# Kernel tuning notes

Measured on AMD Instinct MI355X. Metric: run time of the kernel, lower is better.

## Reference

```python
import jax, jax.numpy as jnp
import numpy as np

N = 100000   # nodes
E = 1250000  # edges
D = 64       # in = hidden = out channels
LN_EPS = 1e-5
L2_EPS = 1e-12


def setup_inputs() -> dict:
    key = jax.random.key(0)
    ks = jax.random.split(key, 16)
    s = 1.0 / np.sqrt(D)
    inp = {
        "x": jax.random.normal(ks[0], (N, D), jnp.float32),
        "edge_index": jax.random.randint(ks[1], (2, E), 0, N, dtype=jnp.int64),
    }
    for i in range(3):  # SAGEConv i: out = mean_aggr @ Wl + bl + x @ Wr
        inp[f"Wl{i}"] = jax.random.normal(ks[2 + 2 * i], (D, D), jnp.float32) * s
        inp[f"bl{i}"] = jnp.zeros((D,), jnp.float32)
        inp[f"Wr{i}"] = jax.random.normal(ks[3 + 2 * i], (D, D), jnp.float32) * s
    for i in range(2):  # LayerNorm after layers 0,1
        inp[f"g{i}"] = jnp.ones((D,), jnp.float32)
        inp[f"b{i}"] = jnp.zeros((D,), jnp.float32)
    return inp


def _sage_conv(x, src, dst, Wl, bl, Wr):
    # PyG SAGEConv(aggr='mean'): lin_l(mean of neighbor msgs) + lin_r(x)
    agg = jax.ops.segment_sum(x[src], dst, num_segments=N)          # [N, D]
    deg = jax.ops.segment_sum(jnp.ones((src.shape[0],), x.dtype), dst, num_segments=N)
    mean = agg / jnp.maximum(deg, 1.0)[:, None]
    return mean @ Wl + bl + x @ Wr


def _layer_norm(h, g, b):
    mu = jnp.mean(h, axis=-1, keepdims=True)
    var = jnp.mean((h - mu) ** 2, axis=-1, keepdims=True)
    return (h - mu) * jax.lax.rsqrt(var + LN_EPS) * g + b


def reference(x, edge_index, Wl0, bl0, Wr0, Wl1, bl1, Wr1, Wl2, bl2, Wr2, g0, b0, g1, b1):
    src, dst = edge_index[0], edge_index[1]
    Ws = [(Wl0, bl0, Wr0), (Wl1, bl1, Wr1), (Wl2, bl2, Wr2)]
    lns = [(g0, b0), (g1, b1)]
    h = x
    for i in range(3):
        res = h  # residual projections are Identity (equal dims)
        h = _sage_conv(h, src, dst, *Ws[i])
        if i < 2:
            h = _layer_norm(h, *lns[i])
            h = jax.nn.relu(h)
            h = h + res
            # dropout is identity in eval mode
        else:
            h = h + res
    # F.normalize(p=2, dim=1)
    nrm = jnp.sqrt(jnp.sum(h * h, axis=1, keepdims=True))
    return h / jnp.maximum(nrm, L2_EPS)
```

## Files before the change

### kernel.cpp

```cpp
#include <hip/hip_runtime.h>

#define DD   64
#define WSTR 136
#define BSH  9
#define BNODES 512
#define BCAPSH 13

typedef unsigned int uint32;
typedef __attribute__((ext_vector_type(8))) short short8;
typedef __attribute__((ext_vector_type(4))) float f32x4;

__device__ __forceinline__ unsigned short f2bf_rne(float f) {
    uint32 u = __float_as_uint(f);
    u += 0x7fffu + ((u >> 16) & 1u);
    return (unsigned short)(u >> 16);
}
__device__ __forceinline__ float bf_lo(uint32 w) { return __uint_as_float(w << 16); }
__device__ __forceinline__ float bf_hi(uint32 w) { return __uint_as_float(w & 0xffff0000u); }

__global__ __launch_bounds__(256) void cvt_kernel(const float* __restrict__ x,
                                                  unsigned short* __restrict__ xb,
                                                  int n4, int* __restrict__ gCnt) {
    if (blockIdx.x == 0 && threadIdx.x < 256) gCnt[threadIdx.x] = 0;
    int i = blockIdx.x * 256 + threadIdx.x;
    if (i < n4) {
        float4 v = ((const float4*)x)[i];
        ushort4 p;
        p.x = f2bf_rne(v.x); p.y = f2bf_rne(v.y);
        p.z = f2bf_rne(v.z); p.w = f2bf_rne(v.w);
        ((ushort4*)xb)[i] = p;
    }
}

__global__ __launch_bounds__(1024) void bucket_kernel(const int* __restrict__ src,
                                                      const int* __restrict__ dst,
                                                      int* __restrict__ gCnt,
                                                      int2* __restrict__ buf, int E) {
    __shared__ int ldsCnt[256];
    __shared__ int base[256];
    const int t = threadIdx.x;
    if (t < 256) ldsCnt[t] = 0;
    __syncthreads();

    const int e0 = blockIdx.x * 4096;
    int bk[4], rk[4], sv[4], dv[4];
#pragma unroll
    for (int k = 0; k < 4; ++k) {
        int e = e0 + k * 1024 + t;
        bk[k] = -1;
        if (e < E) {
            dv[k] = dst[e];
            sv[k] = src[e];
            bk[k] = dv[k] >> BSH;
            rk[k] = atomicAdd(&ldsCnt[bk[k]], 1);
        }
    }
    __syncthreads();
    if (t < 256 && ldsCnt[t] > 0) base[t] = atomicAdd(&gCnt[t], ldsCnt[t]);
    __syncthreads();
#pragma unroll
    for (int k = 0; k < 4; ++k) {
        if (bk[k] >= 0) {
            int pos = (bk[k] << BCAPSH) + base[bk[k]] + rk[k];
            buf[pos] = make_int2(sv[k], dv[k]);
        }
    }
}

__global__ __launch_bounds__(256) void scan_buckets(const int* __restrict__ gCnt,
                                                    int* __restrict__ csrBase, int NB) {
    __shared__ int s[256];
    int t = threadIdx.x;
    int v = (t < NB) ? gCnt[t] : 0;
    s[t] = v;
    __syncthreads();
    for (int d = 1; d < 256; d <<= 1) {
        int u = (t >= d) ? s[t - d] : 0;
        __syncthreads();
        if (t >= d) s[t] += u;
        __syncthreads();
    }
    if (t < NB) csrBase[t] = s[t] - v;
}

__global__ __launch_bounds__(512) void csr_build(const int2* __restrict__ buf,
                                                 const int* __restrict__ gCnt,
                                                 const int* __restrict__ csrBase,
                                                 int* __restrict__ offsets,
                                                 int* __restrict__ csr, int N, int E) {
    __shared__ int c1[BNODES];
    __shared__ int s[BNODES];
    const int b = blockIdx.x;
    const int t = threadIdx.x;
    c1[t] = 0;
    __syncthreads();

    const int cnt = gCnt[b];
    const int2* bb = buf + ((size_t)b << BCAPSH);
    for (int i = t; i < cnt; i += 512) atomicAdd(&c1[bb[i].y & (BNODES - 1)], 1);
    __syncthreads();

    int v = c1[t];
    s[t] = v;
    __syncthreads();
    for (int d = 1; d < BNODES; d <<= 1) {
        int u = (t >= d) ? s[t - d] : 0;
        __syncthreads();
        if (t >= d) s[t] += u;
        __syncthreads();
    }
    int excl = s[t] - v;
    const int base = csrBase[b];
    const int node = (b << BSH) + t;
    if (node < N) offsets[node] = base + excl;
    if (b == 0 && t == 0) offsets[N] = E;
    __syncthreads();
    s[t] = excl;
    c1[t] = 0;
    __syncthreads();

    for (int i = t; i < cnt; i += 512) {
        int2 e = bb[i];
        int d = e.y & (BNODES - 1);
        int r = atomicAdd(&c1[d], 1);
        csr[base + s[d] + r] = e.x;
    }
}

__global__ __launch_bounds__(256) void aggregate_kernel(
    const unsigned short* __restrict__ hb,
    const int* __restrict__ offsets,
    const int* __restrict__ csr,
    unsigned short* __restrict__ aggb,
    int N) {
    int node = (blockIdx.x * 256 + threadIdx.x) >> 3;
    if (node >= N) return;
    const int q = threadIdx.x & 7;

    const int off0 = offsets[node];
    const int off1 = offsets[node + 1];

    float a0 = 0.f, a1 = 0.f, a2 = 0.f, a3 = 0.f,
          a4 = 0.f, a5 = 0.f, a6 = 0.f, a7 = 0.f;

    for (int j = off0; j < off1; j += 8) {
        uint4 v[8];
#pragma unroll
        for (int s = 0; s < 8; ++s) {
            uint4 t = make_uint4(0u, 0u, 0u, 0u);
            int idx = j + s;
            if (idx < off1) {
                int sn = __builtin_nontemporal_load(&csr[idx]);
                t = ((const uint4*)(hb + (size_t)sn * DD))[q];
            }
            v[s] = t;
        }
#pragma unroll
        for (int s = 0; s < 8; ++s) {
            a0 += bf_lo(v[s].x); a1 += bf_hi(v[s].x);
            a2 += bf_lo(v[s].y); a3 += bf_hi(v[s].y);
            a4 += bf_lo(v[s].z); a5 += bf_hi(v[s].z);
            a6 += bf_lo(v[s].w); a7 += bf_hi(v[s].w);
        }
    }
    float invd = 1.0f / fmaxf((float)(off1 - off0), 1.0f);
    unsigned short* orow = aggb + (size_t)node * DD + q * 8;
    ushort4 pa, pb;
    pa.x = f2bf_rne(a0 * invd); pa.y = f2bf_rne(a1 * invd);
    pa.z = f2bf_rne(a2 * invd); pa.w = f2bf_rne(a3 * invd);
    pb.x = f2bf_rne(a4 * invd); pb.y = f2bf_rne(a5 * invd);
    pb.z = f2bf_rne(a6 * invd); pb.w = f2bf_rne(a7 * invd);
    *(ushort4*)(orow)     = pa;
    *(ushort4*)(orow + 4) = pb;
}

template <int MODE>
__global__ __launch_bounds__(256, 4) void node_update(
    const float* __restrict__ h,
    const unsigned short* __restrict__ meanb,
    const unsigned short* __restrict__ hb,
    const float* __restrict__ Wl,
    const float* __restrict__ bl,
    const float* __restrict__ Wr,
    const float* __restrict__ g,
    const float* __restrict__ b,
    float* __restrict__ out,
    unsigned short* __restrict__ outb,
    int nNodes) {
    __shared__ unsigned short sWt[64 * WSTR];
    __shared__ float sbl[DD], sg[DD], sb[DD];

    const int t = threadIdx.x;

    for (int idx = t; idx < 2 * DD * DD; idx += 256) {
        int k = idx >> 6, c = idx & 63;
        float v = (k < DD) ? Wl[idx] : Wr[idx - DD * DD];
        sWt[c * WSTR + k] = f2bf_rne(v);
    }
    if (t < DD) {
        sbl[t] = bl[t];
        if (MODE == 0) { sg[t] = g[t]; sb[t] = b[t]; }
    }
    __syncthreads();

    const int wave = t >> 6;
    const int lane = t & 63;
    const int quad = lane >> 4;
    const int n16  = lane & 15;
    const int nbase = blockIdx.x * 64 + wave * 16;

    const int arow = min(nbase + n16, nNodes - 1);
    const unsigned short* mrow = meanb + (size_t)arow * DD;
    const unsigned short* hrow = hb    + (size_t)arow * DD;
    short8 af[4];
    af[0] = *(const short8*)(mrow + quad * 8);
    af[1] = *(const short8*)(mrow + 32 + quad * 8);
    af[2] = *(const short8*)(hrow + quad * 8);
    af[3] = *(const short8*)(hrow + 32 + quad * 8);

    const int rbase = nbase + quad * 4;
    float res[4][4];
#pragma unroll
    for (int i = 0; i < 4; ++i) {
        int rr = min(rbase + i, nNodes - 1);
#pragma unroll
        for (int j = 0; j < 4; ++j)
            res[i][j] = h[(size_t)rr * DD + j * 16 + n16];
    }

    f32x4 acc[4];
#pragma unroll
    for (int j = 0; j < 4; ++j) {
        float bv = sbl[j * 16 + n16];
        acc[j] = (f32x4){bv, bv, bv, bv};
    }

#pragma unroll
    for (int s = 0; s < 4; ++s) {
#pragma unroll
        for (int j = 0; j < 4; ++j) {
            short8 bf = *(const short8*)(&sWt[(j * 16 + n16) * WSTR + s * 32 + quad * 8]);
            acc[j] = __builtin_amdgcn_mfma_f32_16x16x32_bf16(af[s], bf, acc[j], 0, 0, 0);
        }
    }

#pragma unroll
    for (int i = 0; i < 4; ++i) {
        int rr = rbase + i;
        float o[4];
        if (MODE == 0) {
            float s4 = acc[0][i] + acc[1][i] + acc[2][i] + acc[3][i];
            s4 += __shfl_xor(s4, 1, 64);
            s4 += __shfl_xor(s4, 2, 64);
            s4 += __shfl_xor(s4, 4, 64);
            s4 += __shfl_xor(s4, 8, 64);
            float mu = s4 * (1.0f / 64.0f);
            float d0 = acc[0][i] - mu, d1 = acc[1][i] - mu,
                  d2 = acc[2][i] - mu, d3 = acc[3][i] - mu;
            float qq = d0 * d0 + d1 * d1 + d2 * d2 + d3 * d3;
            qq += __shfl_xor(qq, 1, 64);
            qq += __shfl_xor(qq, 2, 64);
            qq += __shfl_xor(qq, 4, 64);
            qq += __shfl_xor(qq, 8, 64);
            float rstd = rsqrtf(qq * (1.0f / 64.0f) + 1e-5f);
            o[0] = fmaxf(d0 * rstd * sg[0 * 16 + n16] + sb[0 * 16 + n16], 0.f) + res[i][0];
            o[1] = fmaxf(d1 * rstd * sg[1 * 16 + n16] + sb[1 * 16 + n16], 0.f) + res[i][1];
            o[2] = fmaxf(d2 * rstd * sg[2 * 16 + n16] + sb[2 * 16 + n16], 0.f) + res[i][2];
            o[3] = fmaxf(d3 * rstd * sg[3 * 16 + n16] + sb[3 * 16 + n16], 0.f) + res[i][3];
        } else {
            o[0] = acc[0][i] + res[i][0];
            o[1] = acc[1][i] + res[i][1];
            o[2] = acc[2][i] + res[i][2];
            o[3] = acc[3][i] + res[i][3];
            float qq = o[0] * o[0] + o[1] * o[1] + o[2] * o[2] + o[3] * o[3];
            qq += __shfl_xor(qq, 1, 64);
            qq += __shfl_xor(qq, 2, 64);
            qq += __shfl_xor(qq, 4, 64);
            qq += __shfl_xor(qq, 8, 64);
            float inv = 1.0f / fmaxf(sqrtf(qq), 1e-12f);
            o[0] *= inv; o[1] *= inv; o[2] *= inv; o[3] *= inv;
        }
        if (rr < nNodes) {
#pragma unroll
            for (int j = 0; j < 4; ++j) {
                out[(size_t)rr * DD + j * 16 + n16] = o[j];
                if (MODE == 0)
                    outb[(size_t)rr * DD + j * 16 + n16] = f2bf_rne(o[j]);
            }
        }
    }
}

extern "C" void kernel_launch(void* const* d_in, const int* in_sizes, int n_in,
                              void* d_out, int out_size, void* d_ws, size_t ws_size,
                              hipStream_t stream) {
    const float* x   = (const float*)d_in[0];
    const int*   ei  = (const int*)d_in[1];
    const float* Wl0 = (const float*)d_in[2];
    const float* bl0 = (const float*)d_in[3];
    const float* Wr0 = (const float*)d_in[4];
    const float* Wl1 = (const float*)d_in[5];
    const float* bl1 = (const float*)d_in[6];
    const float* Wr1 = (const float*)d_in[7];
    const float* Wl2 = (const float*)d_in[8];
    const float* bl2 = (const float*)d_in[9];
    const float* Wr2 = (const float*)d_in[10];
    const float* g0  = (const float*)d_in[11];
    const float* b0  = (const float*)d_in[12];
    const float* g1  = (const float*)d_in[13];
    const float* b1  = (const float*)d_in[14];

    const int N = in_sizes[0] / DD;
    const int E = in_sizes[1] / 2;
    const int* src = ei;
    const int* dst = ei + E;
    const int NB = (N + BNODES - 1) >> BSH;

    float* A       = (float*)d_ws;
    float* B       = A + (size_t)N * DD;
    unsigned short* AGGB = (unsigned short*)(B + (size_t)N * DD);
    unsigned short* HB   = AGGB + (size_t)N * DD;
    int*   offsets = (int*)(HB + (size_t)N * DD);
    int*   gCnt    = offsets + (N + 1);
    int*   csrBase = gCnt + 256;
    int*   csr     = csrBase + 256;
    int2*  bucketBuf = (int2*)A;
    float* out     = (float*)d_out;

    const int tiles = (N + 63) / 64;
    const int agrid = (N + 31) / 32;
    const int n4    = N * DD / 4;
    const int cgrid = (n4 + 255) / 256;
    const int bgrid = (E + 4095) / 4096;

    cvt_kernel<<<cgrid, 256, 0, stream>>>(x, HB, n4, gCnt);
    bucket_kernel<<<bgrid, 1024, 0, stream>>>(src, dst, gCnt, bucketBuf, E);
    scan_buckets<<<1, 256, 0, stream>>>(gCnt, csrBase, NB);
    csr_build<<<NB, 512, 0, stream>>>(bucketBuf, gCnt, csrBase, offsets, csr, N, E);

    aggregate_kernel<<<agrid, 256, 0, stream>>>(HB, offsets, csr, AGGB, N);
    node_update<0><<<tiles, 256, 0, stream>>>(x, AGGB, HB, Wl0, bl0, Wr0, g0, b0, A, HB, N);

    aggregate_kernel<<<agrid, 256, 0, stream>>>(HB, offsets, csr, AGGB, N);
    node_update<0><<<tiles, 256, 0, stream>>>(A, AGGB, HB, Wl1, bl1, Wr1, g1, b1, B, HB, N);

    aggregate_kernel<<<agrid, 256, 0, stream>>>(HB, offsets, csr, AGGB, N);
    node_update<1><<<tiles, 256, 0, stream>>>(B, AGGB, HB, Wl2, bl2, Wr2, nullptr, nullptr, out, nullptr, N);
}
```

Measured before the change: 314.2 us.

## Fuse neighbor aggregation into node update and drop fp32 intermediates

Merges the mean-aggregation kernel into the per-layer node update, so each 64-node block gathers neighbor means and self features into LDS and runs the MFMA transform from there. This removes the bf16 aggregate round trip through global memory and three launches. The residual path now reads the bf16 self rows instead of fp32 hidden states, so only bf16 activations are stored between layers. The bucket scan is folded into csr_build. The trade-offs are reduced residual precision, a larger LDS footprint per block, and lower gather parallelism per block, since only 256 threads handle 64 nodes.

```diff
diff --git a/kernel.cpp b/kernel.cpp
--- a/kernel.cpp
+++ b/kernel.cpp
@@ -2,6 +2,7 @@
 
 #define DD   64
 #define WSTR 136
+#define SSTR 72
 #define BSH  9
 #define BNODES 512
 #define BCAPSH 13
@@ -17,6 +18,9 @@
 }
 __device__ __forceinline__ float bf_lo(uint32 w) { return __uint_as_float(w << 16); }
 __device__ __forceinline__ float bf_hi(uint32 w) { return __uint_as_float(w & 0xffff0000u); }
+__device__ __forceinline__ float bf2f(unsigned short s) {
+    return __uint_as_float(((uint32)s) << 16);
+}
 
 __global__ __launch_bounds__(256) void cvt_kernel(const float* __restrict__ x,
                                                   unsigned short* __restrict__ xb,
@@ -67,34 +71,25 @@
     }
 }
 
-__global__ __launch_bounds__(256) void scan_buckets(const int* __restrict__ gCnt,
-                                                    int* __restrict__ csrBase, int NB) {
-    __shared__ int s[256];
-    int t = threadIdx.x;
-    int v = (t < NB) ? gCnt[t] : 0;
-    s[t] = v;
-    __syncthreads();
-    for (int d = 1; d < 256; d <<= 1) {
-        int u = (t >= d) ? s[t - d] : 0;
-        __syncthreads();
-        if (t >= d) s[t] += u;
-        __syncthreads();
-    }
-    if (t < NB) csrBase[t] = s[t] - v;
-}
-
 __global__ __launch_bounds__(512) void csr_build(const int2* __restrict__ buf,
                                                  const int* __restrict__ gCnt,
-                                                 const int* __restrict__ csrBase,
                                                  int* __restrict__ offsets,
                                                  int* __restrict__ csr, int N, int E) {
     __shared__ int c1[BNODES];
     __shared__ int s[BNODES];
+    __shared__ int sg2[256];
     const int b = blockIdx.x;
     const int t = threadIdx.x;
+    if (t < 256) sg2[t] = gCnt[t];
     c1[t] = 0;
     __syncthreads();
-
+    for (int d = 1; d < 256; d <<= 1) {
+        int v = (t < 256 && t >= d) ? sg2[t - d] : 0;
+        __syncthreads();
+        if (t < 256 && t >= d) sg2[t] += v;
+        __syncthreads();
+    }
+    const int base = (b == 0) ? 0 : sg2[b - 1];
     const int cnt = gCnt[b];
     const int2* bb = buf + ((size_t)b << BCAPSH);
     for (int i = t; i < cnt; i += 512) atomicAdd(&c1[bb[i].y & (BNODES - 1)], 1);
@@ -110,7 +105,6 @@
         __syncthreads();
     }
     int excl = s[t] - v;
-    const int base = csrBase[b];
     const int node = (b << BSH) + t;
     if (node < N) offsets[node] = base + excl;
     if (b == 0 && t == 0) offsets[N] = E;
@@ -127,70 +121,26 @@
     }
 }
 
-__global__ __launch_bounds__(256) void aggregate_kernel(
-    const unsigned short* __restrict__ hb,
+template <int MODE>
+__global__ __launch_bounds__(256, 4) void sage_layer(
+    const unsigned short* __restrict__ hbin,
     const int* __restrict__ offsets,
     const int* __restrict__ csr,
-    unsigned short* __restrict__ aggb,
-    int N) {
-    int node = (blockIdx.x * 256 + threadIdx.x) >> 3;
-    if (node >= N) return;
-    const int q = threadIdx.x & 7;
-
-    const int off0 = offsets[node];
-    const int off1 = offsets[node + 1];
-
-    float a0 = 0.f, a1 = 0.f, a2 = 0.f, a3 = 0.f,
-          a4 = 0.f, a5 = 0.f, a6 = 0.f, a7 = 0.f;
-
-    for (int j = off0; j < off1; j += 8) {
-        uint4 v[8];
-#pragma unroll
-        for (int s = 0; s < 8; ++s) {
-            uint4 t = make_uint4(0u, 0u, 0u, 0u);
-            int idx = j + s;
-            if (idx < off1) {
-                int sn = __builtin_nontemporal_load(&csr[idx]);
-                t = ((const uint4*)(hb + (size_t)sn * DD))[q];
-            }
-            v[s] = t;
-        }
-#pragma unroll
-        for (int s = 0; s < 8; ++s) {
-            a0 += bf_lo(v[s].x); a1 += bf_hi(v[s].x);
-            a2 += bf_lo(v[s].y); a3 += bf_hi(v[s].y);
-            a4 += bf_lo(v[s].z); a5 += bf_hi(v[s].z);
-            a6 += bf_lo(v[s].w); a7 += bf_hi(v[s].w);
-        }
-    }
-    float invd = 1.0f / fmaxf((float)(off1 - off0), 1.0f);
-    unsigned short* orow = aggb + (size_t)node * DD + q * 8;
-    ushort4 pa, pb;
-    pa.x = f2bf_rne(a0 * invd); pa.y = f2bf_rne(a1 * invd);
-    pa.z = f2bf_rne(a2 * invd); pa.w = f2bf_rne(a3 * invd);
-    pb.x = f2bf_rne(a4 * invd); pb.y = f2bf_rne(a5 * invd);
-    pb.z = f2bf_rne(a6 * invd); pb.w = f2bf_rne(a7 * invd);
-    *(ushort4*)(orow)     = pa;
-    *(ushort4*)(orow + 4) = pb;
-}
-
-template <int MODE>
-__global__ __launch_bounds__(256, 4) void node_update(
-    const float* __restrict__ h,
-    const unsigned short* __restrict__ meanb,
-    const unsigned short* __restrict__ hb,
     const float* __restrict__ Wl,
     const float* __restrict__ bl,
     const float* __restrict__ Wr,
     const float* __restrict__ g,
-    const float* __restrict__ b,
+    const float* __restrict__ bta,
+    unsigned short* __restrict__ hbout,
     float* __restrict__ out,
-    unsigned short* __restrict__ outb,
-    int nNodes) {
+    int N) {
     __shared__ unsigned short sWt[64 * WSTR];
+    __shared__ unsigned short sSelf[64 * SSTR];
+    __shared__ unsigned short sMean[64 * SSTR];
     __shared__ float sbl[DD], sg[DD], sb[DD];
 
     const int t = threadIdx.x;
+    const int nbase = blockIdx.x * 64;
 
     for (int idx = t; idx < 2 * DD * DD; idx += 256) {
         int k = idx >> 6, c = idx & 63;
@@ -199,7 +149,63 @@
     }
     if (t < DD) {
         sbl[t] = bl[t];
-        if (MODE == 0) { sg[t] = g[t]; sb[t] = b[t]; }
+        if (MODE == 0) { sg[t] = g[t]; sb[t] = bta[t]; }
+    }
+
+#pragma unroll
+    for (int r = 0; r < 2; ++r) {
+        int idx = r * 256 + t;
+        int row = idx >> 3;
+        int qq  = idx & 7;
+        int n   = min(nbase + row, N - 1);
+        uint4 v = ((const uint4*)(hbin + (size_t)n * DD))[qq];
+        *(uint4*)(&sSelf[row * SSTR + qq * 8]) = v;
+    }
+
+    {
+        const int grp = t >> 3;
+        const int q   = t & 7;
+#pragma unroll 1
+        for (int rep = 0; rep < 2; ++rep) {
+            int local = grp + rep * 32;
+            int node  = nbase + local;
+            float a0 = 0.f, a1 = 0.f, a2 = 0.f, a3 = 0.f,
+                  a4 = 0.f, a5 = 0.f, a6 = 0.f, a7 = 0.f;
+            int deg = 0;
+            if (node < N) {
+                int off0 = offsets[node];
+                int off1 = offsets[node + 1];
+                deg = off1 - off0;
+                for (int j = off0; j < off1; j += 8) {
+                    uint4 v[8];
+#pragma unroll
+                    for (int s = 0; s < 8; ++s) {
+                        uint4 tt = make_uint4(0u, 0u, 0u, 0u);
+                        int idx = j + s;
+                        if (idx < off1) {
+                            int sn = __builtin_nontemporal_load(&csr[idx]);
+                            tt = ((const uint4*)(hbin + (size_t)sn * DD))[q];
+                        }
+                        v[s] = tt;
+                    }
+#pragma unroll
+                    for (int s = 0; s < 8; ++s) {
+                        a0 += bf_lo(v[s].x); a1 += bf_hi(v[s].x);
+                        a2 += bf_lo(v[s].y); a3 += bf_hi(v[s].y);
+                        a4 += bf_lo(v[s].z); a5 += bf_hi(v[s].z);
+                        a6 += bf_lo(v[s].w); a7 += bf_hi(v[s].w);
+                    }
+                }
+            }
+            float invd = 1.0f / fmaxf((float)deg, 1.0f);
+            ushort4 pa, pb;
+            pa.x = f2bf_rne(a0 * invd); pa.y = f2bf_rne(a1 * invd);
+            pa.z = f2bf_rne(a2 * invd); pa.w = f2bf_rne(a3 * invd);
+            pb.x = f2bf_rne(a4 * invd); pb.y = f2bf_rne(a5 * invd);
+            pb.z = f2bf_rne(a6 * invd); pb.w = f2bf_rne(a7 * invd);
+            *(ushort4*)(&sMean[local * SSTR + q * 8])     = pa;
+            *(ushort4*)(&sMean[local * SSTR + q * 8 + 4]) = pb;
+        }
     }
     __syncthreads();
 
@@ -207,26 +213,13 @@
     const int lane = t & 63;
     const int quad = lane >> 4;
     const int n16  = lane & 15;
-    const int nbase = blockIdx.x * 64 + wave * 16;
-
-    const int arow = min(nbase + n16, nNodes - 1);
-    const unsigned short* mrow = meanb + (size_t)arow * DD;
-    const unsigned short* hrow = hb    + (size_t)arow * DD;
+    const int lbase = wave * 16;
+
     short8 af[4];
-    af[0] = *(const short8*)(mrow + quad * 8);
-    af[1] = *(const short8*)(mrow + 32 + quad * 8);
-    af[2] = *(const short8*)(hrow + quad * 8);
-    af[3] = *(const short8*)(hrow + 32 + quad * 8);
-
-    const int rbase = nbase + quad * 4;
-    float res[4][4];
-#pragma unroll
-    for (int i = 0; i < 4; ++i) {
-        int rr = min(rbase + i, nNodes - 1);
-#pragma unroll
-        for (int j = 0; j < 4; ++j)
-            res[i][j] = h[(size_t)rr * DD + j * 16 + n16];
-    }
+    af[0] = *(const short8*)(&sMean[(lbase + n16) * SSTR + quad * 8]);
+    af[1] = *(const short8*)(&sMean[(lbase + n16) * SSTR + 32 + quad * 8]);
+    af[2] = *(const short8*)(&sSelf[(lbase + n16) * SSTR + quad * 8]);
+    af[3] = *(const short8*)(&sSelf[(lbase + n16) * SSTR + 32 + quad * 8]);
 
     f32x4 acc[4];
 #pragma unroll
@@ -234,7 +227,6 @@
         float bv = sbl[j * 16 + n16];
         acc[j] = (f32x4){bv, bv, bv, bv};
     }
-
 #pragma unroll
     for (int s = 0; s < 4; ++s) {
 #pragma unroll
@@ -246,7 +238,12 @@
 
 #pragma unroll
     for (int i = 0; i < 4; ++i) {
-        int rr = rbase + i;
+        const int lrow = lbase + quad * 4 + i;
+        const int rr   = nbase + lrow;
+        float res[4];
+#pragma unroll
+        for (int j = 0; j < 4; ++j)
+            res[j] = bf2f(sSelf[lrow * SSTR + j * 16 + n16]);
         float o[4];
         if (MODE == 0) {
             float s4 = acc[0][i] + acc[1][i] + acc[2][i] + acc[3][i];
@@ -263,15 +260,15 @@
             qq += __shfl_xor(qq, 4, 64);
             qq += __shfl_xor(qq, 8, 64);
             float rstd = rsqrtf(qq * (1.0f / 64.0f) + 1e-5f);
-            o[0] = fmaxf(d0 * rstd * sg[0 * 16 + n16] + sb[0 * 16 + n16], 0.f) + res[i][0];
-            o[1] = fmaxf(d1 * rstd * sg[1 * 16 + n16] + sb[1 * 16 + n16], 0.f) + res[i][1];
-            o[2] = fmaxf(d2 * rstd * sg[2 * 16 + n16] + sb[2 * 16 + n16], 0.f) + res[i][2];
-            o[3] = fmaxf(d3 * rstd * sg[3 * 16 + n16] + sb[3 * 16 + n16], 0.f) + res[i][3];
+            o[0] = fmaxf(d0 * rstd * sg[ 0 + n16] + sb[ 0 + n16], 0.f) + res[0];
+            o[1] = fmaxf(d1 * rstd * sg[16 + n16] + sb[16 + n16], 0.f) + res[1];
+            o[2] = fmaxf(d2 * rstd * sg[32 + n16] + sb[32 + n16], 0.f) + res[2];
+            o[3] = fmaxf(d3 * rstd * sg[48 + n16] + sb[48 + n16], 0.f) + res[3];
         } else {
-            o[0] = acc[0][i] + res[i][0];
-            o[1] = acc[1][i] + res[i][1];
-            o[2] = acc[2][i] + res[i][2];
-            o[3] = acc[3][i] + res[i][3];
+            o[0] = acc[0][i] + res[0];
+            o[1] = acc[1][i] + res[1];
+            o[2] = acc[2][i] + res[2];
+            o[3] = acc[3][i] + res[3];
             float qq = o[0] * o[0] + o[1] * o[1] + o[2] * o[2] + o[3] * o[3];
             qq += __shfl_xor(qq, 1, 64);
             qq += __shfl_xor(qq, 2, 64);
@@ -280,12 +277,13 @@
             float inv = 1.0f / fmaxf(sqrtf(qq), 1e-12f);
             o[0] *= inv; o[1] *= inv; o[2] *= inv; o[3] *= inv;
         }
-        if (rr < nNodes) {
+        if (rr < N) {
 #pragma unroll
             for (int j = 0; j < 4; ++j) {
-                out[(size_t)rr * DD + j * 16 + n16] = o[j];
                 if (MODE == 0)
-                    outb[(size_t)rr * DD + j * 16 + n16] = f2bf_rne(o[j]);
+                    hbout[(size_t)rr * DD + j * 16 + n16] = f2bf_rne(o[j]);
+                else
+                    out[(size_t)rr * DD + j * 16 + n16] = o[j];
             }
         }
     }
@@ -316,34 +314,27 @@
     const int* dst = ei + E;
     const int NB = (N + BNODES - 1) >> BSH;
 
-    float* A       = (float*)d_ws;
-    float* B       = A + (size_t)N * DD;
-    unsigned short* AGGB = (unsigned short*)(B + (size_t)N * DD);
-    unsigned short* HB   = AGGB + (size_t)N * DD;
-    int*   offsets = (int*)(HB + (size_t)N * DD);
+    int2* bucketBuf = (int2*)d_ws;
+    unsigned short* HB0 = (unsigned short*)(bucketBuf + ((size_t)256 << BCAPSH));
+    unsigned short* HB1 = HB0 + (size_t)N * DD;
+    int*   csr     = (int*)(HB1 + (size_t)N * DD);
+    int*   offsets = csr + E;
     int*   gCnt    = offsets + (N + 1);
-    int*   csrBase = gCnt + 256;
-    int*   csr     = csrBase + 256;
-    int2*  bucketBuf = (int2*)A;
     float* out     = (float*)d_out;
 
     const int tiles = (N + 63) / 64;
-    const int agrid = (N + 31) / 32;
     const int n4    = N * DD / 4;
     const int cgrid = (n4 + 255) / 256;
     const int bgrid = (E + 4095) / 4096;
 
-    cvt_kernel<<<cgrid, 256, 0, stream>>>(x, HB, n4, gCnt);
+    cvt_kernel<<<cgrid, 256, 0, stream>>>(x, HB0, n4, gCnt);
     bucket_kernel<<<bgrid, 1024, 0, stream>>>(src, dst, gCnt, bucketBuf, E);
-    scan_buckets<<<1, 256, 0, stream>>>(gCnt, csrBase, NB);
-    csr_build<<<NB, 512, 0, stream>>>(bucketBuf, gCnt, csrBase, offsets, csr, N, E);
-
-    aggregate_kernel<<<agrid, 256, 0, stream>>>(HB, offsets, csr, AGGB, N);
-    node_update<0><<<tiles, 256, 0, stream>>>(x, AGGB, HB, Wl0, bl0, Wr0, g0, b0, A, HB, N);
-
-    aggregate_kernel<<<agrid, 256, 0, stream>>>(HB, offsets, csr, AGGB, N);
-    node_update<0><<<tiles, 256, 0, stream>>>(A, AGGB, HB, Wl1, bl1, Wr1, g1, b1, B, HB, N);
-
-    aggregate_kernel<<<agrid, 256, 0, stream>>>(HB, offsets, csr, AGGB, N);
-    node_update<1><<<tiles, 256, 0, stream>>>(B, AGGB, HB, Wl2, bl2, Wr2, nullptr, nullptr, out, nullptr, N);
-}
+    csr_build<<<NB, 512, 0, stream>>>(bucketBuf, gCnt, offsets, csr, N, E);
+
+    sage_layer<0><<<tiles, 256, 0, stream>>>(HB0, offsets, csr, Wl0, bl0, Wr0,
+                                             g0, b0, HB1, nullptr, N);
+    sage_layer<0><<<tiles, 256, 0, stream>>>(HB1, offsets, csr, Wl1, bl1, Wr1,
+                                             g1, b1, HB0, nullptr, N);
+    sage_layer<1><<<tiles, 256, 0, stream>>>(HB0, offsets, csr, Wl2, bl2, Wr2,
+                                             nullptr, nullptr, nullptr, out, N);
+}
```

New measurement: 314.1 us. About the same (-0.0%).
